# Optimization experiments

Measured on AMD Instinct MI355X. Metric: run time of the kernel, lower is better.

## Reference

```python
import jax, jax.numpy as jnp
import numpy as np
import math

D = 2048      # hidden_size
H = 16        # num_heads
DH = 128      # head_dim
RQ = 1024     # q_rank
RK = 512      # kv_rank
B, T = 2, 2048

def setup_inputs() -> dict:
    key = jax.random.key(0)
    ks = jax.random.split(key, 8)
    s = lambda fan_in: 1.0 / math.sqrt(fan_in)
    return {
        "x": jax.random.normal(ks[0], (B, T, D), dtype=jnp.float32),
        "Wq_down": jax.random.normal(ks[1], (RQ, D), dtype=jnp.float32) * s(D),
        "Wkv_down": jax.random.normal(ks[2], (RK, D), dtype=jnp.float32) * s(D),
        "Wq_up": jax.random.normal(ks[3], (D, RQ), dtype=jnp.float32) * s(RQ),
        "Wk_up": jax.random.normal(ks[4], (D, RK), dtype=jnp.float32) * s(RK),
        "Wv_up": jax.random.normal(ks[5], (D, RK), dtype=jnp.float32) * s(RK),
        "Wo": jax.random.normal(ks[6], (D, D), dtype=jnp.float32) * s(D),
        "bo": jnp.zeros((D,), dtype=jnp.float32),
    }

def _heads_view(w, rank):
    # w: [H*DH, rank] -> [H, rank, DH]  (matches torch view(H,DH,r).transpose(1,2))
    return w.reshape(H, DH, rank).transpose(0, 2, 1)

def reference(x, Wq_down, Wkv_down, Wq_up, Wk_up, Wv_up, Wo, bo):
    Bx, Tx, d = x.shape
    # low-rank down-projections (torch Linear: x @ W.T)
    Q_lat = x @ Wq_down.T            # [B,T,RQ]
    C_kv = x @ Wkv_down.T            # [B,S,RK]  (S == T, no cache)
    S = C_kv.shape[1]
    # absorbed score matrix M = Uq Uk^T / sqrt(d_h): [H,RQ,RK]
    Uq_h = _heads_view(Wq_up, RQ)    # [H,RQ,DH]
    Uk_h = _heads_view(Wk_up, RK)    # [H,RK,DH]
    Mmat = jnp.einsum('hqd,hkd->hqk', Uq_h, Uk_h) * (1.0 / math.sqrt(DH))
    # logits in latent space: [B,H,T,S]
    logits = jnp.einsum('btq,hqk,bsk->bhts', Q_lat, Mmat, C_kv)
    # causal mask (P = S - T = 0)
    P = S - Tx
    i = jnp.arange(Tx)[:, None]
    j = jnp.arange(S)[None, :]
    neg_inf = jnp.float32(-jnp.inf)
    logits = jnp.where((j > P + i)[None, None], neg_inf, logits)
    # fp32 softmax (every causal row has >=1 valid key, no NaNs)
    attn = jax.nn.softmax(logits.astype(jnp.float32), axis=-1).astype(x.dtype)
    # value up-projection per head: [B,H,S,DH]
    Uv_h = _heads_view(Wv_up, RK)    # [H,RK,DH]
    V_up = jnp.einsum('bsr,hrd->bhsd', C_kv, Uv_h)
    ctx = jnp.einsum('bhts,bhsd->bhtd', attn, V_up)      # [B,H,T,DH]
    ctx = ctx.transpose(0, 2, 1, 3).reshape(Bx, Tx, H * DH)
    out = ctx @ Wo.T + bo
    return out
```

## Files before the change

### kernel.cpp

```cpp
#include <hip/hip_runtime.h>

typedef __bf16 bf16x8 __attribute__((ext_vector_type(8)));
typedef float f32x4 __attribute__((ext_vector_type(4)));
typedef float f32x16 __attribute__((ext_vector_type(16)));
typedef unsigned short u16x4 __attribute__((ext_vector_type(4)));
typedef unsigned int u32x4 __attribute__((ext_vector_type(4)));

#define L2E 1.44269504088896340736f

__device__ __forceinline__ f32x4 mfma16(bf16x8 a, bf16x8 b, f32x4 c) {
  return __builtin_amdgcn_mfma_f32_16x16x32_bf16(a, b, c, 0, 0, 0);
}
__device__ __forceinline__ f32x16 mfma32(bf16x8 a, bf16x8 b, f32x16 c) {
  return __builtin_amdgcn_mfma_f32_32x32x16_bf16(a, b, c, 0, 0, 0);
}

__device__ __forceinline__ void async16(const __bf16* g, __bf16* l) {
  __builtin_amdgcn_global_load_lds(
      (const __attribute__((address_space(1))) void*)g,
      (__attribute__((address_space(3))) void*)l, 16, 0, 0);
}

__device__ __forceinline__ unsigned pk(float x, float y) {
  unsigned short lo = __builtin_bit_cast(unsigned short, (__bf16)x);
  unsigned short hi = __builtin_bit_cast(unsigned short, (__bf16)y);
  return ((unsigned)hi << 16) | (unsigned)lo;
}

__global__ __launch_bounds__(256) void cvt_all(
    const float* __restrict__ x, const float* __restrict__ wqd,
    const float* __restrict__ wkvd, const float* __restrict__ wqup,
    const float* __restrict__ wkup, const float* __restrict__ wvup,
    const float* __restrict__ wo, __bf16* __restrict__ dx,
    __bf16* __restrict__ dqkv, __bf16* __restrict__ dqu,
    __bf16* __restrict__ dku, __bf16* __restrict__ dvu,
    __bf16* __restrict__ dwo) {
  int bx = blockIdx.x;
  const float* s;
  __bf16* d;
  int off;
  if (bx < 8192)       { s = x;    d = dx;                 off = bx; }
  else if (bx < 10240) { s = wqd;  d = dqkv;               off = bx - 8192; }
  else if (bx < 11264) { s = wkvd; d = dqkv + 1024 * 2048; off = bx - 10240; }
  else if (bx < 13312) { s = wqup; d = dqu;                off = bx - 11264; }
  else if (bx < 14336) { s = wkup; d = dku;                off = bx - 13312; }
  else if (bx < 15360) { s = wvup; d = dvu;                off = bx - 14336; }
  else                 { s = wo;   d = dwo;                off = bx - 15360; }
  long i = (long)off * 1024 + threadIdx.x * 4;
  f32x4 v = *(const f32x4*)(s + i);
  u16x4 o;
#pragma unroll
  for (int j = 0; j < 4; j++) o[j] = __builtin_bit_cast(unsigned short, (__bf16)v[j]);
  *(u16x4*)((unsigned short*)d + i) = o;
}

template <int OUTF32>
__device__ __forceinline__ void gemm_body(
    __bf16* As, __bf16* Bs, const __bf16* __restrict__ A,
    const __bf16* __restrict__ Bt, void* __restrict__ Cout,
    const float* __restrict__ bias, int lda, int ldb, int ldc, int N, int K,
    float scale, int bx, int by, int permn) {
  const int tid = threadIdx.x;
  const int wid = tid >> 6, lane = tid & 63;
  const int lrow = lane & 15, lkhi = lane >> 4;
  const int row0 = bx * 128, col0 = by * 128;
  const int wr = (wid >> 1) * 64, wc = (wid & 1) * 64;

  const int trow = tid >> 3;
  const int scol = 8 * ((tid & 7) ^ (trow & 7));
  const __bf16* pA = A + (size_t)(row0 + trow) * lda + scol;
  const __bf16* pB = Bt + (size_t)(col0 + trow) * ldb + scol;

  f32x4 acc[4][4] = {};
  for (int k0 = 0; k0 < K; k0 += 64) {
    __syncthreads();
#pragma unroll
    for (int p = 0; p < 4; p++)
      async16(pA + (size_t)(32 * p) * lda, As + p * 2048 + wid * 512);
#pragma unroll
    for (int p = 0; p < 4; p++)
      async16(pB + (size_t)(32 * p) * ldb, Bs + p * 2048 + wid * 512);
    pA += 64; pB += 64;
    __syncthreads();
#pragma unroll
    for (int kk = 0; kk < 2; kk++) {
      bf16x8 af[4], bv[4];
#pragma unroll
      for (int mi = 0; mi < 4; mi++) {
        int rr = wr + mi * 16 + lrow;
        af[mi] = *(const bf16x8*)(As + rr * 64 +
                                  ((kk * 32 + lkhi * 8) ^ (8 * (rr & 7))));
      }
#pragma unroll
      for (int ni = 0; ni < 4; ni++) {
        int rr = wc + ni * 16 + lrow;
        bv[ni] = *(const bf16x8*)(Bs + rr * 64 +
                                  ((kk * 32 + lkhi * 8) ^ (8 * (rr & 7))));
      }
#pragma unroll
      for (int mi = 0; mi < 4; mi++)
#pragma unroll
        for (int ni = 0; ni < 4; ni++)
          acc[mi][ni] = mfma16(af[mi], bv[ni], acc[mi][ni]);
    }
  }

  const int orow = row0 + wr + lkhi * 4;
  const int prow = permn ? ((lrow & 3) | ((lrow & 4) << 1) | ((lrow & 8) >> 1))
                         : lrow;
  const int ocol = col0 + wc + prow;
#pragma unroll
  for (int mi = 0; mi < 4; mi++)
#pragma unroll
    for (int ni = 0; ni < 4; ni++)
#pragma unroll
      for (int r = 0; r < 4; r++) {
        size_t idx = (size_t)(orow + mi * 16 + r) * ldc + (ocol + ni * 16);
        float v = acc[mi][ni][r] * scale;
        if (OUTF32)
          ((float*)Cout)[idx] = v + bias[ocol + ni * 16];
        else
          ((__bf16*)Cout)[idx] = (__bf16)v;
      }
}

template <int OUTF32, int PERMN = 0>
__global__ __launch_bounds__(256, 3) void gemm_bt(
    const __bf16* __restrict__ A, const __bf16* __restrict__ Bt,
    void* __restrict__ Cout, const float* __restrict__ bias,
    int lda, int ldb, int ldc, int N, int K, float scale) {
  __shared__ __align__(16) __bf16 As[8192];
  __shared__ __align__(16) __bf16 Bs[8192];
  gemm_body<OUTF32>(As, Bs, A, Bt, Cout, bias, lda, ldb, ldc, N, K, scale,
                    blockIdx.x, blockIdx.y, PERMN);
}

__global__ __launch_bounds__(256, 3) void gemm_mid(
    const __bf16* __restrict__ qlat, const __bf16* __restrict__ ckv,
    const __bf16* __restrict__ wqu, const __bf16* __restrict__ wku,
    const __bf16* __restrict__ wvu, __bf16* __restrict__ qf,
    __bf16* __restrict__ kf, __bf16* __restrict__ vt) {
  __shared__ __align__(16) __bf16 As[8192];
  __shared__ __align__(16) __bf16 Bs[8192];
  int bid = (int)blockIdx.x;
  if (bid < 512) {
    gemm_body<0>(As, Bs, qlat, wqu, qf, nullptr, 1536, 1024, 2048, 2048, 1024,
                 0.12752039360437355f, bid & 31, bid >> 5, 0);
  } else if (bid < 1024) {
    bid -= 512;
    gemm_body<0>(As, Bs, ckv, wku, kf, nullptr, 1536, 512, 2048, 2048, 512,
                 1.0f, bid & 31, bid >> 5, 0);
  } else {
    bid -= 1024;
    gemm_body<0>(As, Bs, wvu, ckv, vt, nullptr, 512, 1536, 4096, 4096, 512,
                 1.0f, bid & 15, bid >> 4, 1);
  }
}

__global__ __launch_bounds__(512, 1) void mla_attn(
    const __bf16* __restrict__ Qf, const __bf16* __restrict__ Kf,
    const __bf16* __restrict__ Vt, __bf16* __restrict__ ctx) {
  __shared__ __align__(16) __bf16 SM[2][32768];
  __shared__ float MLl[128];

  const int bid = (int)blockIdx.x;
  const int qt = 15 - (bid >> 5);
  const int bh = bid & 31;
  const int h = bh >> 1, b = bh & 1;
  const int tid = threadIdx.x;
  const int half = tid >> 8;
  const int htid = tid & 255;
  const int wid4 = htid >> 6;
  const int lane = tid & 63;
  const int l31 = lane & 31;
  const bool hh = (lane & 32) != 0;

  __bf16* Ks = &SM[half][0];
  __bf16* Vs = &SM[half][16384];

  const __bf16* Kbh = Kf + (size_t)b * 2048 * 2048 + h * 128;
  const __bf16* Vbh = Vt + (size_t)h * 128 * 4096 + b * 2048;

  auto stage = [&](int k0, int buf) {
#pragma unroll
    for (int i = 0; i < 4; i++) {
      int e = i * 2048 + htid * 8;
      int krow = e >> 7;
      int kcol = (e & 127) ^ (8 * (krow & 15));
      async16(Kbh + (size_t)(k0 + krow) * 2048 + kcol,
              Ks + buf * 8192 + i * 2048 + wid4 * 512);
    }
#pragma unroll
    for (int i = 0; i < 4; i++) {
      int e = i * 2048 + htid * 8;
      int vrow = e >> 6;
      int vcol = (e & 63) ^ (8 * (vrow & 7));
      async16(Vbh + (size_t)vrow * 4096 + k0 + vcol,
              Vs + buf * 8192 + i * 2048 + wid4 * 512);
    }
  };

  const int q0 = qt * 128;
  const int ntile = qt + 1;
  const int kbase = half * ntile;
  const int q = q0 + wid4 * 32 + l31;

  bf16x8 qb[8];
  const __bf16* qrow =
      Qf + (size_t)(b * 2048 + q) * 2048 + h * 128 + (hh ? 8 : 0);
#pragma unroll
  for (int ds = 0; ds < 8; ds++) qb[ds] = *(const bf16x8*)(qrow + ds * 16);

  f32x16 o[4] = {};
  float lsum = 0.f;

  int cur = 0;
  stage(kbase * 64, 0);

  for (int t = 0; t < ntile; t++) {
    const int kb = kbase + t;
    const int k0 = kb * 64;
    __syncthreads();
    if (t + 1 < ntile) stage(k0 + 64, cur ^ 1);

    f32x16 sa[2] = {}, sb[2] = {};
    __builtin_amdgcn_s_setprio(1);
#pragma unroll
    for (int ds = 0; ds < 4; ds++) {
#pragma unroll
      for (int kt = 0; kt < 2; kt++) {
        int row = kt * 32 + l31;
        int col = (ds * 16 + (hh ? 8 : 0)) ^ (8 * (row & 15));
        bf16x8 kfr = *(const bf16x8*)(Ks + cur * 8192 + row * 128 + col);
        sa[kt] = mfma32(kfr, qb[ds], sa[kt]);
      }
    }
#pragma unroll
    for (int ds = 4; ds < 8; ds++) {
#pragma unroll
      for (int kt = 0; kt < 2; kt++) {
        int row = kt * 32 + l31;
        int col = (ds * 16 + (hh ? 8 : 0)) ^ (8 * (row & 15));
        bf16x8 kfr = *(const bf16x8*)(Ks + cur * 8192 + row * 128 + col);
        sb[kt] = mfma32(kfr, qb[ds], sb[kt]);
      }
    }
    __builtin_amdgcn_s_setprio(0);
    f32x16 sacc[2];
    sacc[0] = sa[0] + sb[0];
    sacc[1] = sa[1] + sb[1];

    if (kb >= 2 * qt) {
#pragma unroll
      for (int kt = 0; kt < 2; kt++)
#pragma unroll
        for (int r = 0; r < 16; r++) {
          int key = k0 + kt * 32 + (r & 3) + 8 * (r >> 2) + (hh ? 4 : 0);
          if (key > q) sacc[kt][r] = -1e30f;
        }
    }

    float ps0 = 0.f, ps1 = 0.f, ps2 = 0.f, ps3 = 0.f;
#pragma unroll
    for (int kt = 0; kt < 2; kt++)
#pragma unroll
      for (int r = 0; r < 16; r += 4) {
        float a0 = __builtin_amdgcn_exp2f(sacc[kt][r + 0]);
        float a1 = __builtin_amdgcn_exp2f(sacc[kt][r + 1]);
        float a2 = __builtin_amdgcn_exp2f(sacc[kt][r + 2]);
        float a3 = __builtin_amdgcn_exp2f(sacc[kt][r + 3]);
        sacc[kt][r + 0] = a0; sacc[kt][r + 1] = a1;
        sacc[kt][r + 2] = a2; sacc[kt][r + 3] = a3;
        ps0 += a0; ps1 += a1; ps2 += a2; ps3 += a3;
      }

    __builtin_amdgcn_s_setprio(1);
#pragma unroll
    for (int s = 0; s < 4; s++) {
      const int kt = s >> 1, r8 = (s & 1) * 8;
      u32x4 wv;
      wv.x = pk(sacc[kt][r8 + 0], sacc[kt][r8 + 1]);
      wv.y = pk(sacc[kt][r8 + 2], sacc[kt][r8 + 3]);
      wv.z = pk(sacc[kt][r8 + 4], sacc[kt][r8 + 5]);
      wv.w = pk(sacc[kt][r8 + 6], sacc[kt][r8 + 7]);
      bf16x8 pa = __builtin_bit_cast(bf16x8, wv);
#pragma unroll
      for (int dt = 0; dt < 4; dt++) {
        int vrow = dt * 32 + l31;
        int vcol = (s * 16 + (hh ? 8 : 0)) ^ (8 * (vrow & 7));
        bf16x8 vf = *(const bf16x8*)(Vs + cur * 8192 + vrow * 64 + vcol);
        o[dt] = mfma32(pa, vf, o[dt]);
      }
    }
    __builtin_amdgcn_s_setprio(0);

    float ps = (ps0 + ps1) + (ps2 + ps3);
    ps += __shfl_xor(ps, 32);
    lsum += ps;
    cur ^= 1;
  }

  __syncthreads();
  float* om = (float*)&SM[1][0];
  if (half == 1) {
#pragma unroll
    for (int dt = 0; dt < 4; dt++) {
      int base = ((wid4 * 4 + dt) * 64 + lane) * 16;
#pragma unroll
      for (int r = 0; r < 16; r++) om[base + r] = o[dt][r];
    }
    if (!hh) MLl[wid4 * 32 + l31] = lsum;
  }
  __syncthreads();
  if (half == 0) {
#pragma unroll
    for (int r = 0; r < 16; r++) {
      int ql = (r & 3) + 8 * (r >> 2) + (hh ? 4 : 0);
      float l0r = __shfl(lsum, ql);
      float l1r = MLl[wid4 * 32 + ql];
      float inv = 1.f / (l0r + l1r);
      size_t rowi = (size_t)(b * 2048 + q0 + wid4 * 32 + ql) * 2048 + h * 128;
#pragma unroll
      for (int dt = 0; dt < 4; dt++) {
        float o1v = om[((wid4 * 4 + dt) * 64 + lane) * 16 + r];
        ctx[rowi + dt * 32 + l31] = (__bf16)((o[dt][r] + o1v) * inv);
      }
    }
  }
}

extern "C" void kernel_launch(void* const* d_in, const int* in_sizes, int n_in,
                              void* d_out, int out_size, void* d_ws, size_t ws_size,
                              hipStream_t stream) {
  (void)in_sizes; (void)n_in; (void)out_size; (void)ws_size;
  const float* x    = (const float*)d_in[0];
  const float* wqd  = (const float*)d_in[1];
  const float* wkvd = (const float*)d_in[2];
  const float* wqup = (const float*)d_in[3];
  const float* wkup = (const float*)d_in[4];
  const float* wvup = (const float*)d_in[5];
  const float* wo   = (const float*)d_in[6];
  const float* bo   = (const float*)d_in[7];

  char* ws = (char*)d_ws;
  const size_t MB = 1024 * 1024;
  __bf16* x_bf     = (__bf16*)(ws + 0);
  __bf16* q_full   = (__bf16*)(ws + 16 * MB);
  __bf16* k_full   = (__bf16*)(ws + 32 * MB);
  __bf16* vt       = (__bf16*)(ws + 48 * MB);
  __bf16* qkv_lat  = (__bf16*)(ws + 64 * MB);
  __bf16* wqkvd_bf = (__bf16*)(ws + 76 * MB);
  __bf16* wqup_bf  = (__bf16*)(ws + 82 * MB);
  __bf16* wkup_bf  = (__bf16*)(ws + 86 * MB);
  __bf16* wvup_bf  = (__bf16*)(ws + 88 * MB);
  __bf16* wo_bf    = (__bf16*)(ws + 90 * MB);
  __bf16* ctx = x_bf;

  cvt_all<<<19456, 256, 0, stream>>>(x, wqd, wkvd, wqup, wkup, wvup, wo, x_bf,
                                     wqkvd_bf, wqup_bf, wkup_bf, wvup_bf,
                                     wo_bf);

  dim3 blk(256);
  gemm_bt<0><<<dim3(32, 12), blk, 0, stream>>>(x_bf, wqkvd_bf, qkv_lat, nullptr,
                                               2048, 2048, 1536, 1536, 2048, 1.0f);
  gemm_mid<<<1536, blk, 0, stream>>>(qkv_lat, qkv_lat + 1024, wqup_bf, wkup_bf,
                                     wvup_bf, q_full, k_full, vt);
  mla_attn<<<512, 512, 0, stream>>>(q_full, k_full, vt, ctx);
  gemm_bt<1><<<dim3(32, 16), blk, 0, stream>>>(ctx, wo_bf, (float*)d_out, bo,
                                               2048, 2048, 2048, 2048, 2048, 1.0f);
}
```

Measured before the change: 187.6 us.

## Split weight conversions and fold them into later GEMM launches to overlap

The single fp32-to-bf16 conversion kernel is split up. Only x and the down-projection weights are converted before the first GEMM. The up-projection weight conversions ride as extra blocks inside the down-projection GEMM launch, and the Wo conversion rides inside the mid GEMM launch. This lets memory-bound conversion work overlap with compute-bound GEMM blocks and removes it from the critical path before the first GEMM. The risk is that mixed block types in one launch can cause tail or scheduling imbalance.

```diff
diff --git a/kernel.cpp b/kernel.cpp
--- a/kernel.cpp
+++ b/kernel.cpp
@@ -27,31 +27,24 @@
   return ((unsigned)hi << 16) | (unsigned)lo;
 }
 
-__global__ __launch_bounds__(256) void cvt_all(
-    const float* __restrict__ x, const float* __restrict__ wqd,
-    const float* __restrict__ wkvd, const float* __restrict__ wqup,
-    const float* __restrict__ wkup, const float* __restrict__ wvup,
-    const float* __restrict__ wo, __bf16* __restrict__ dx,
-    __bf16* __restrict__ dqkv, __bf16* __restrict__ dqu,
-    __bf16* __restrict__ dku, __bf16* __restrict__ dvu,
-    __bf16* __restrict__ dwo) {
-  int bx = blockIdx.x;
-  const float* s;
-  __bf16* d;
-  int off;
-  if (bx < 8192)       { s = x;    d = dx;                 off = bx; }
-  else if (bx < 10240) { s = wqd;  d = dqkv;               off = bx - 8192; }
-  else if (bx < 11264) { s = wkvd; d = dqkv + 1024 * 2048; off = bx - 10240; }
-  else if (bx < 13312) { s = wqup; d = dqu;                off = bx - 11264; }
-  else if (bx < 14336) { s = wkup; d = dku;                off = bx - 13312; }
-  else if (bx < 15360) { s = wvup; d = dvu;                off = bx - 14336; }
-  else                 { s = wo;   d = dwo;                off = bx - 15360; }
+__device__ __forceinline__ void cvt_chunk(const float* __restrict__ s,
+                                          __bf16* __restrict__ d, int off) {
   long i = (long)off * 1024 + threadIdx.x * 4;
   f32x4 v = *(const f32x4*)(s + i);
   u16x4 o;
 #pragma unroll
   for (int j = 0; j < 4; j++) o[j] = __builtin_bit_cast(unsigned short, (__bf16)v[j]);
   *(u16x4*)((unsigned short*)d + i) = o;
+}
+
+__global__ __launch_bounds__(256) void cvt_pre(
+    const float* __restrict__ x, const float* __restrict__ wqd,
+    const float* __restrict__ wkvd, __bf16* __restrict__ dx,
+    __bf16* __restrict__ dqkv) {
+  int bx = blockIdx.x;
+  if (bx < 8192)       cvt_chunk(x, dx, bx);
+  else if (bx < 10240) cvt_chunk(wqd, dqkv, bx - 8192);
+  else                 cvt_chunk(wkvd, dqkv + 1024 * 2048, bx - 10240);
 }
 
 template <int OUTF32>
@@ -135,11 +128,33 @@
                     blockIdx.x, blockIdx.y, PERMN);
 }
 
-__global__ __launch_bounds__(256, 3) void gemm_mid(
+__global__ __launch_bounds__(256, 3) void gemm_down_fused(
+    const __bf16* __restrict__ xbf, const __bf16* __restrict__ wqkvd,
+    __bf16* __restrict__ qkvlat, const float* __restrict__ wqup,
+    const float* __restrict__ wkup, const float* __restrict__ wvup,
+    __bf16* __restrict__ dqu, __bf16* __restrict__ dku,
+    __bf16* __restrict__ dvu) {
+  __shared__ __align__(16) __bf16 As[8192];
+  __shared__ __align__(16) __bf16 Bs[8192];
+  int bid = (int)blockIdx.x;
+  if (bid < 384) {
+    gemm_body<0>(As, Bs, xbf, wqkvd, qkvlat, nullptr, 2048, 2048, 1536, 1536,
+                 2048, 1.0f, bid & 31, bid >> 5, 0);
+  } else if (bid < 2432) {
+    cvt_chunk(wqup, dqu, bid - 384);
+  } else if (bid < 3456) {
+    cvt_chunk(wkup, dku, bid - 2432);
+  } else {
+    cvt_chunk(wvup, dvu, bid - 3456);
+  }
+}
+
+__global__ __launch_bounds__(256, 3) void gemm_mid_fused(
     const __bf16* __restrict__ qlat, const __bf16* __restrict__ ckv,
     const __bf16* __restrict__ wqu, const __bf16* __restrict__ wku,
     const __bf16* __restrict__ wvu, __bf16* __restrict__ qf,
-    __bf16* __restrict__ kf, __bf16* __restrict__ vt) {
+    __bf16* __restrict__ kf, __bf16* __restrict__ vt,
+    const float* __restrict__ wo, __bf16* __restrict__ dwo) {
   __shared__ __align__(16) __bf16 As[8192];
   __shared__ __align__(16) __bf16 Bs[8192];
   int bid = (int)blockIdx.x;
@@ -150,10 +165,12 @@
     bid -= 512;
     gemm_body<0>(As, Bs, ckv, wku, kf, nullptr, 1536, 512, 2048, 2048, 512,
                  1.0f, bid & 31, bid >> 5, 0);
-  } else {
+  } else if (bid < 1536) {
     bid -= 1024;
     gemm_body<0>(As, Bs, wvu, ckv, vt, nullptr, 512, 1536, 4096, 4096, 512,
                  1.0f, bid & 15, bid >> 4, 1);
+  } else {
+    cvt_chunk(wo, dwo, bid - 1536);
   }
 }
 
@@ -356,15 +373,14 @@
   __bf16* wo_bf    = (__bf16*)(ws + 90 * MB);
   __bf16* ctx = x_bf;
 
-  cvt_all<<<19456, 256, 0, stream>>>(x, wqd, wkvd, wqup, wkup, wvup, wo, x_bf,
-                                     wqkvd_bf, wqup_bf, wkup_bf, wvup_bf,
-                                     wo_bf);
-
   dim3 blk(256);
-  gemm_bt<0><<<dim3(32, 12), blk, 0, stream>>>(x_bf, wqkvd_bf, qkv_lat, nullptr,
-                                               2048, 2048, 1536, 1536, 2048, 1.0f);
-  gemm_mid<<<1536, blk, 0, stream>>>(qkv_lat, qkv_lat + 1024, wqup_bf, wkup_bf,
-                                     wvup_bf, q_full, k_full, vt);
+  cvt_pre<<<11264, blk, 0, stream>>>(x, wqd, wkvd, x_bf, wqkvd_bf);
+  gemm_down_fused<<<4480, blk, 0, stream>>>(x_bf, wqkvd_bf, qkv_lat, wqup,
+                                            wkup, wvup, wqup_bf, wkup_bf,
+                                            wvup_bf);
+  gemm_mid_fused<<<5632, blk, 0, stream>>>(qkv_lat, qkv_lat + 1024, wqup_bf,
+                                           wkup_bf, wvup_bf, q_full, k_full,
+                                           vt, wo, wo_bf);
   mla_attn<<<512, 512, 0, stream>>>(q_full, k_full, vt, ctx);
   gemm_bt<1><<<dim3(32, 16), blk, 0, stream>>>(ctx, wo_bf, (float*)d_out, bo,
                                                2048, 2048, 2048, 2048, 2048, 1.0f);
```

Measured after the change: 183.0 us. 2.5% less time.
